# Kernel tuning notes

Measured on AMD Instinct MI355X. Metric: run time of the kernel, lower is better.

The kernel has to match this reference:

```python
import jax, jax.numpy as jnp
import numpy as np
from jax import lax

# ---- constants matching init kwargs / proposal_creator(mode='testing') ----
RATIOS = (0.5, 1.0, 2.0)
SCALES = (8.0, 16.0, 32.0)
BASE = 16.0          # generate_anchor_base base_size
STRIDE = 16          # feat_stride
NMS_THRESH = 0.7
N_PRE = 3000         # n_test_pre_nms
N_POST = 300         # n_test_post_nms
MIN_SIZE = 16.0      # min_size * scale (scale=1)


def _anchor_base():
    # (9, 4) xyxy anchors centered at (BASE/2, BASE/2); ratios outer, scales inner
    r = np.array(RATIOS, np.float32)
    s = np.array(SCALES, np.float32)
    hs = (BASE * s[None, :] * np.sqrt(r)[:, None]).reshape(-1)
    ws = (BASE * s[None, :] * np.sqrt(1.0 / r)[:, None]).reshape(-1)
    cx = cy = BASE / 2.0
    return np.stack([cx - ws / 2, cy - hs / 2, cx + ws / 2, cy + hs / 2], 1).astype(np.float32)


def _all_anchors(h, w):
    # _enumerate_shifted_anchor: shift grid flattened y-outer/x-inner to match
    # permute(0,2,3,1).view(n,-1,4) layout of the conv outputs.
    base = jnp.asarray(_anchor_base())                     # (9,4)
    sx = jnp.arange(w, dtype=jnp.float32) * STRIDE
    sy = jnp.arange(h, dtype=jnp.float32) * STRIDE
    SX, SY = jnp.meshgrid(sx, sy)                          # (h,w)
    shifts = jnp.stack([SX, SY, SX, SY], -1).reshape(-1, 4)  # (h*w,4)
    return (shifts[:, None, :] + base[None, :, :]).reshape(-1, 4)  # (h*w*9,4)


def _proposals(loc, score, anchor, img_h, img_w):
    # loc: (K,4) deltas, score: (K,) fg prob, anchor: (K,4) xyxy
    aw = anchor[:, 2] - anchor[:, 0]
    ah = anchor[:, 3] - anchor[:, 1]
    acx = anchor[:, 0] + 0.5 * aw
    acy = anchor[:, 1] + 0.5 * ah
    cx = loc[:, 0] * aw + acx
    cy = loc[:, 1] * ah + acy
    bw = aw * jnp.exp(loc[:, 2])
    bh = ah * jnp.exp(loc[:, 3])
    x1 = jnp.clip(cx - 0.5 * bw, 0.0, img_w)
    y1 = jnp.clip(cy - 0.5 * bh, 0.0, img_h)
    x2 = jnp.clip(cx + 0.5 * bw, 0.0, img_w)
    y2 = jnp.clip(cy + 0.5 * bh, 0.0, img_h)
    boxes = jnp.stack([x1, y1, x2, y2], 1)
    valid = ((x2 - x1) >= MIN_SIZE) & ((y2 - y1) >= MIN_SIZE)
    # min-size filter -> sink invalid boxes with -inf score, then top-k pre-NMS
    masked = jnp.where(valid, score, -jnp.inf)
    _, idx = lax.top_k(masked, N_PRE)
    b = boxes[idx]                                         # (N_PRE,4), score-sorted desc
    v = valid[idx]
    # pairwise IoU (torchvision convention: no +1)
    area = (b[:, 2] - b[:, 0]) * (b[:, 3] - b[:, 1])
    ix1 = jnp.maximum(b[:, None, 0], b[None, :, 0])
    iy1 = jnp.maximum(b[:, None, 1], b[None, :, 1])
    ix2 = jnp.minimum(b[:, None, 2], b[None, :, 2])
    iy2 = jnp.minimum(b[:, None, 3], b[None, :, 3])
    inter = jnp.clip(ix2 - ix1, 0.0) * jnp.clip(iy2 - iy1, 0.0)
    union = area[:, None] + area[None, :] - inter
    iou = jnp.where(union > 0.0, inter / union, 0.0)
    sup = iou > NMS_THRESH                                 # (N_PRE,N_PRE) bool
    # greedy sequential NMS over score order
    ar = jnp.arange(N_PRE)
    def body(keep, i):
        keep = keep & ~(keep[i] & sup[i] & (ar > i))
        return keep, None
    keep, _ = lax.scan(body, v, ar)
    # first N_POST kept boxes (score order); pad by cycling kept boxes
    order = jnp.argsort(jnp.where(keep, ar, N_PRE))        # kept indices first, sorted
    nk = jnp.maximum(keep.sum(), 1)
    pos = jnp.arange(N_POST)
    sel = order[jnp.where(pos < nk, pos, pos % nk)]
    return b[sel]                                          # (N_POST,4)


def setup_inputs() -> dict:
    key = jax.random.key(0)
    ks = jax.random.split(key, 4)
    n, c, h, w = 4, 512, 38, 38
    return {
        "x": jax.random.normal(ks[0], (n, c, h, w), jnp.float32),
        "conv1_w": jax.random.normal(ks[1], (512, 512, 3, 3), jnp.float32) * 0.01,
        "conv1_b": jnp.zeros((512,), jnp.float32),
        "score_w": jax.random.normal(ks[2], (18, 512), jnp.float32) * 0.01,
        "score_b": jnp.zeros((18,), jnp.float32),
        "loc_w": jax.random.normal(ks[3], (36, 512), jnp.float32) * 0.01,
        "loc_b": jnp.zeros((36,), jnp.float32),
        "img_h": 608,
        "img_w": 608,
    }


def reference(x, conv1_w, conv1_b, score_w, score_b, loc_w, loc_b, img_h, img_w):
    n, _, h, w = x.shape
    feat = jax.nn.relu(
        lax.conv_general_dilated(x, conv1_w, (1, 1), "SAME",
                                 dimension_numbers=("NCHW", "OIHW", "NCHW"))
        + conv1_b[None, :, None, None])
    locs = jnp.einsum("nchw,oc->nohw", feat, loc_w) + loc_b[None, :, None, None]
    scores = jnp.einsum("nchw,oc->nohw", feat, score_w) + score_b[None, :, None, None]
    rpn_locs = locs.transpose(0, 2, 3, 1).reshape(n, -1, 4)      # (n, h*w*9, 4)
    rpn_scores = scores.transpose(0, 2, 3, 1).reshape(n, -1, 2)  # (n, h*w*9, 2)
    fg = jax.nn.softmax(rpn_scores, axis=-1)[..., 1]             # (n, h*w*9)
    anchor = _all_anchors(h, w)
    ih = jnp.float32(img_h)
    iw = jnp.float32(img_w)
    rois = jax.vmap(lambda l, s: _proposals(l, s, anchor, ih, iw))(rpn_locs, fg)
    rois_indices = jnp.broadcast_to(
        jnp.arange(n, dtype=x.dtype)[:, None], (n, N_POST))
    return rpn_locs, rpn_scores, rois.reshape(-1, 4), rois_indices, anchor[None]
```

## Files before the change

### kernel.cpp

```cpp
#include <hip/hip_runtime.h>
#include <cstdint>
#include <cstddef>

#define HW    1444
#define NA    12996
#define NPRE  3000
#define NW    47
#define NPOST 300

#define OFF_LOCS   0
#define OFF_SCORES 207936
#define OFF_ROIS   311904
#define OFF_IDX    316704
#define OFF_ANCH   317904

#define INVALID_KEY 0xFFF0000000000000ULL

typedef float f32x2 __attribute__((ext_vector_type(2)));

__device__ inline double as_dim(int raw) {
  if (raw > 0 && raw < 1000000) return (double)raw;
  return (double)__int_as_float(raw);
}

__global__ __launch_bounds__(256) void wt_k(const float* __restrict__ lw,
                                            const float* __restrict__ sw,
                                            float* __restrict__ Wt) {
  int t = blockIdx.x * 256 + threadIdx.x;
  if (t >= 64 * 512) return;
  int o = t & 63, c = t >> 6;
  float v = 0.f;
  if (o < 36)      v = lw[o * 512 + c];
  else if (o < 54) v = sw[(o - 36) * 512 + c];
  Wt[t] = v;
}

__global__ __launch_bounds__(256) void conv_k(const float* __restrict__ X,
                                              const float* __restrict__ W,
                                              const float* __restrict__ B,
                                              float* __restrict__ F) {
  __shared__ float Xs[480];
  __shared__ float Wsf[2340];
  const int tid  = threadIdx.x;
  const int lane = tid & 63;
  const int wv   = tid >> 6;
  const int seg  = wv * 10;
  const int y  = blockIdx.x;
  const int o0 = blockIdx.y * 64;
  const int n  = blockIdx.z;
  const float* xn = X + ((size_t)n * 512) * HW;

  int xsrc[2]; bool xval[2]; bool xact[2];
#pragma unroll
  for (int u = 0; u < 2; ++u) {
    int e = tid + u * 256;
    xact[u] = (e < 480);
    int cl = e / 120, rem = e - cl * 120;
    int row = rem / 40, col = rem - row * 40;
    int iy = y - 1 + row, ix = col - 1;
    xval[u] = xact[u] && (iy >= 0 && iy < 38 && ix >= 0 && ix < 38);
    xsrc[u] = xval[u] ? (cl * HW + iy * 38 + ix) : 0;
  }
  int wdst[9], wsrc[9];
#pragma unroll
  for (int u = 0; u < 9; ++u) {
    int e = tid + u * 256;
    int ol = e / 36, rem = e - ol * 36;
    int cl = rem / 9, k = rem - cl * 9;
    wdst[u] = (cl * 9 + k) * 65 + ol;
    wsrc[u] = (o0 + ol) * 4608 + cl * 9 + k;
  }

  float xr_[2], wr_[9];
#pragma unroll
  for (int u = 0; u < 2; ++u) xr_[u] = xval[u] ? xn[xsrc[u]] : 0.f;
#pragma unroll
  for (int u = 0; u < 9; ++u) wr_[u] = W[wsrc[u]];

  double acc[10];
#pragma unroll
  for (int p = 0; p < 10; ++p) acc[p] = 0.;
  f32x2 pA[5], pB[5];
  float pc0 = 0.f;

  for (int cc = 0; cc < 128; ++cc) {
    __syncthreads();
#pragma unroll
    for (int u = 0; u < 2; ++u)
      if (xact[u]) Xs[tid + u * 256] = xr_[u];
#pragma unroll
    for (int u = 0; u < 9; ++u) Wsf[wdst[u]] = wr_[u];
    __syncthreads();
    if (cc < 127) {
      const int cb = (cc + 1) * 4;
#pragma unroll
      for (int u = 0; u < 2; ++u) xr_[u] = xval[u] ? xn[(size_t)cb * HW + xsrc[u]] : 0.f;
#pragma unroll
      for (int u = 0; u < 9; ++u) wr_[u] = W[wsrc[u] + cb * 9];
    }
    if ((cc & 1) == 0) {
#pragma unroll
      for (int a = 0; a < 5; ++a) { pA[a] = (f32x2)(0.f); pB[a] = (f32x2)(0.f); }
      pc0 = 0.f;
    }
#pragma unroll
    for (int cl = 0; cl < 4; ++cl) {
      f32x2 wp[9];
#pragma unroll
      for (int t = 0; t < 9; ++t) {
        float wv0 = Wsf[(cl * 9 + t) * 65 + lane];
        wp[t][0] = wv0; wp[t][1] = wv0;
      }
#pragma unroll
      for (int ky = 0; ky < 3; ++ky) {
        const float* xrow = &Xs[cl * 120 + ky * 40 + seg];
        f32x2 xp[6];
#pragma unroll
        for (int j = 0; j < 6; ++j) xp[j] = *(const f32x2*)(xrow + 2 * j);
#pragma unroll
        for (int a = 0; a < 5; ++a)
          asm("v_pk_fma_f32 %0, %1, %2, %0"
              : "+v"(pA[a]) : "v"(xp[a]), "v"(wp[ky * 3 + 0]));
        pc0 = fmaf(wp[ky * 3 + 1][0], xp[0][1], pc0);
#pragma unroll
        for (int a = 0; a < 5; ++a)
          asm("v_pk_fma_f32 %0, %1, %2, %0"
              : "+v"(pB[a]) : "v"(xp[a + 1]), "v"(wp[ky * 3 + 1]));
#pragma unroll
        for (int a = 0; a < 5; ++a)
          asm("v_pk_fma_f32 %0, %1, %2, %0"
              : "+v"(pA[a]) : "v"(xp[a + 1]), "v"(wp[ky * 3 + 2]));
      }
    }
    if (cc & 1) {
      acc[0] += (double)(pA[0][0] + pc0);
#pragma unroll
      for (int p = 1; p < 10; ++p) {
        float sa = pA[p >> 1][p & 1];
        float sb = (p & 1) ? pB[(p - 1) >> 1][0] : pB[(p - 2) >> 1][1];
        acc[p] += (double)(sa + sb);
      }
    }
  }
  double bb = (double)B[o0 + lane];
  float* fp = F + ((size_t)(n * 512 + o0 + lane)) * HW + y * 38;
#pragma unroll
  for (int p = 0; p < 10; ++p) {
    int col = seg + p;
    if (col < 38) fp[col] = (float)fmax(acc[p] + bb, 0.0);
  }
}

__global__ __launch_bounds__(256) void heads_k(const float* __restrict__ F,
                                               const float* __restrict__ Wt,
                                               const float* __restrict__ lb,
                                               const float* __restrict__ sb,
                                               float* __restrict__ out,
                                               double* __restrict__ fg) {
  __shared__ float sf[512 * 4];
  __shared__ double ssc[4][18];
  int n = blockIdx.y;
  int p0 = blockIdx.x * 4;
  int tid = threadIdx.x;
  const float* fn = F + ((size_t)n * 512) * HW;
  for (int e = tid; e < 2048; e += 256) {
    int c = e >> 2, pl = e & 3;
    sf[e] = fn[c * HW + p0 + pl];
  }
  __syncthreads();
  int pl = tid & 3, o = tid >> 2;
  double acc = 0.;
  if (o < 54) {
    for (int c = 0; c < 512; ++c)
      acc = fma((double)Wt[(c << 6) | o], (double)sf[(c << 2) | pl], acc);
  }
  int p = p0 + pl;
  if (o < 36) {
    acc += (double)lb[o];
    out[OFF_LOCS + ((size_t)n * NA + (size_t)p * 9 + (o >> 2)) * 4 + (o & 3)] = (float)acc;
  } else if (o < 54) {
    int oo = o - 36;
    acc += (double)sb[oo];
    out[OFF_SCORES + ((size_t)n * NA + (size_t)p * 9 + (oo >> 1)) * 2 + (oo & 1)] = (float)acc;
    ssc[pl][oo] = acc;
  }
  __syncthreads();
  if (tid < 36) {
    int pl2 = tid / 9, a = tid - pl2 * 9;
    double s0 = ssc[pl2][a * 2], s1 = ssc[pl2][a * 2 + 1];
    double mx = fmax(s0, s1);
    double e0 = exp(s0 - mx), e1 = exp(s1 - mx);
    fg[(size_t)n * NA + (size_t)(p0 + pl2) * 9 + a] = e1 / (e0 + e1);
  }
}

__global__ __launch_bounds__(256) void decode_k(const float* __restrict__ out_c,
                                                float* __restrict__ out,
                                                const double* __restrict__ fg,
                                                const int* __restrict__ ihp,
                                                const int* __restrict__ iwp,
                                                double* __restrict__ boxes,
                                                unsigned long long* __restrict__ keys) {
  int t = blockIdx.x * 256 + threadIdx.x;
  int n = t >> 14, i = t & 16383;
  if (i >= NA) { keys[t] = ~0ULL; return; }
  int p = i / 9, a = i - p * 9;
  int ri = a / 3, si = a - ri * 3;
  double sr  = (ri == 0) ? 0.7071067811865476 : (ri == 1 ? 1.0 : 1.4142135623730951);
  double sri = (ri == 0) ? 1.4142135623730951 : (ri == 1 ? 1.0 : 0.7071067811865476);
  double hs = (double)(128 << si) * sr;
  double wd = (double)(128 << si) * sri;
  int py = p / 38, px = p - py * 38;
  float sx = (float)(px * 16), sy = (float)(py * 16);
  float fx1 = (float)(8.0 - 0.5 * wd), fy1 = (float)(8.0 - 0.5 * hs);
  float fx2 = (float)(8.0 + 0.5 * wd), fy2 = (float)(8.0 + 0.5 * hs);
  float ax1f = sx + fx1, ay1f = sy + fy1, ax2f = sx + fx2, ay2f = sy + fy2;
  if (n == 0) {
    float* ap = out + OFF_ANCH + (size_t)i * 4;
    ap[0] = ax1f; ap[1] = ay1f; ap[2] = ax2f; ap[3] = ay2f;
  }
  double ax1 = ax1f, ay1 = ay1f, ax2 = ax2f, ay2 = ay2f;
  double aw = ax2 - ax1, ah = ay2 - ay1;
  double acx = ax1 + 0.5 * aw, acy = ay1 + 0.5 * ah;
  const float* lp = out_c + OFF_LOCS + ((size_t)n * NA + i) * 4;
  double cx = (double)lp[0] * aw + acx, cy = (double)lp[1] * ah + acy;
  double bw = aw * exp((double)lp[2]), bh = ah * exp((double)lp[3]);
  double iwf = as_dim(iwp[0]), ihf = as_dim(ihp[0]);
  double x1 = fmin(fmax(cx - 0.5 * bw, 0.0), iwf);
  double y1 = fmin(fmax(cy - 0.5 * bh, 0.0), ihf);
  double x2 = fmin(fmax(cx + 0.5 * bw, 0.0), iwf);
  double y2 = fmin(fmax(cy + 0.5 * bh, 0.0), ihf);
  bool valid = ((x2 - x1) >= 16.0) && ((y2 - y1) >= 16.0);
  double* bp = boxes + ((size_t)n * NA + i) * 4;
  bp[0] = x1; bp[1] = y1; bp[2] = x2; bp[3] = y2;
  double sc = fg[(size_t)n * NA + i];
  unsigned long long u = (unsigned long long)__double_as_longlong(sc);
  u = (u >> 63) ? ~u : (u | 0x8000000000000000ULL);
  unsigned long long inv = ~u;
  if (!valid) inv = INVALID_KEY;
  keys[t] = (inv & ~0x3FFFULL) | (unsigned long long)i;
}

__global__ __launch_bounds__(1024) void sortA_k(unsigned long long* __restrict__ keys) {
  __shared__ unsigned long long s[8192];
  const int half = blockIdx.x & 1;
  unsigned long long* g = keys + (((size_t)(blockIdx.x >> 1)) << 14) + ((size_t)half << 13);
  const int tid = threadIdx.x;
  for (int i = tid; i < 8192; i += 1024) s[i] = g[i];
  for (int size = 2; size <= 8192; size <<= 1) {
    for (int stride = size >> 1; stride > 0; stride >>= 1) {
      __syncthreads();
      for (int u = tid; u < 4096; u += 1024) {
        int lo = u & (stride - 1);
        int i1 = ((u - lo) << 1) | lo;
        int i2 = i1 + stride;
        bool up = (i1 & size) == 0;
        if (half) up = !up;
        unsigned long long a = s[i1], b = s[i2];
        if ((a > b) == up) { s[i1] = b; s[i2] = a; }
      }
    }
  }
  __syncthreads();
  for (int i = tid; i < 8192; i += 1024) g[i] = s[i];
}

__global__ __launch_bounds__(256) void sortB_k(unsigned long long* __restrict__ keys) {
  int t = blockIdx.x * 256 + threadIdx.x;
  int n = t >> 13, i = t & 8191;
  unsigned long long* g = keys + ((size_t)n << 14);
  unsigned long long a = g[i], b = g[i + 8192];
  if (a > b) { g[i] = b; g[i + 8192] = a; }
}

__global__ __launch_bounds__(1024) void sortC_k(unsigned long long* __restrict__ keys) {
  __shared__ unsigned long long s[8192];
  unsigned long long* g = keys + (((size_t)(blockIdx.x >> 1)) << 14) + ((size_t)(blockIdx.x & 1) << 13);
  const int tid = threadIdx.x;
  for (int i = tid; i < 8192; i += 1024) s[i] = g[i];
  for (int stride = 4096; stride > 0; stride >>= 1) {
    __syncthreads();
    for (int u = tid; u < 4096; u += 1024) {
      int lo = u & (stride - 1);
      int i1 = ((u - lo) << 1) | lo;
      int i2 = i1 + stride;
      unsigned long long a = s[i1], b = s[i2];
      if (a > b) { s[i1] = b; s[i2] = a; }
    }
  }
  __syncthreads();
  for (int i = tid; i < 8192; i += 1024) g[i] = s[i];
}

__global__ void gather_k(const unsigned long long* __restrict__ keys,
                         const double* __restrict__ boxes,
                         double* __restrict__ bsort,
                         unsigned long long* __restrict__ vw) {
  int n = blockIdx.y, w = blockIdx.x, l = threadIdx.x;
  int r = w * 64 + l;
  bool valid = false;
  if (r < NPRE) {
    unsigned long long kk = keys[((size_t)n << 14) + r];
    valid = kk < INVALID_KEY;
    unsigned idx = (unsigned)(kk & 0x3FFFULL);
    const double* bp = boxes + ((size_t)n * NA + idx) * 4;
    double* dp = bsort + ((size_t)n * NPRE + r) * 4;
    dp[0] = bp[0]; dp[1] = bp[1]; dp[2] = bp[2]; dp[3] = bp[3];
  }
  unsigned long long mask = __ballot(valid);
  if (l == 0) vw[n * NW + w] = mask;
}

__global__ __launch_bounds__(256) void iou_k(const double* __restrict__ bsort,
                                             unsigned long long* __restrict__ sup) {
  int t = blockIdx.x * 256 + threadIdx.x;
  if (t >= 4 * NPRE * NW) return;
  int w = t % NW; int rest = t / NW; int i = rest % NPRE; int n = rest / NPRE;
  const double* bb = bsort + (size_t)n * NPRE * 4;
  double bix1 = bb[(size_t)i*4], biy1 = bb[(size_t)i*4+1];
  double bix2 = bb[(size_t)i*4+2], biy2 = bb[(size_t)i*4+3];
  double ai = (bix2 - bix1) * (biy2 - biy1);
  unsigned long long word = 0ULL;
  int j0 = w << 6;
  if (j0 + 63 > i) {
    int lmax = NPRE - j0; if (lmax > 64) lmax = 64;
    for (int l = 0; l < lmax; ++l) {
      int j = j0 + l;
      if (j <= i) continue;
      const double* bj = bb + (size_t)j * 4;
      double aj = (bj[2] - bj[0]) * (bj[3] - bj[1]);
      double xx1 = fmax(bix1, bj[0]), yy1 = fmax(biy1, bj[1]);
      double xx2 = fmin(bix2, bj[2]), yy2 = fmin(biy2, bj[3]);
      double inter = fmax(xx2 - xx1, 0.0) * fmax(yy2 - yy1, 0.0);
      double uni = ai + aj - inter;
      double iou = (uni > 0.0) ? inter / uni : 0.0;
      word |= (unsigned long long)(iou > 0.7) << l;
    }
  }
  sup[((size_t)n * NPRE + i) * NW + w] = word;
}

__global__ void nms_k(const unsigned long long* __restrict__ sup,
                      const unsigned long long* __restrict__ vwp,
                      const double* __restrict__ bsort,
                      float* __restrict__ out) {
  int n = blockIdx.x; int l = threadIdx.x;
  unsigned long long vw = (l < NW) ? vwp[n * NW + l] : 0ULL;
  unsigned long long remv = 0ULL, keepw = 0ULL;
  const unsigned long long* sbase = sup + (size_t)n * NPRE * NW;
  unsigned long long r = (l < NPRE) ? sbase[(size_t)l * NW] : 0ULL;
  for (int b = 0; b < NW; ++b) {
    unsigned long long rn = 0ULL;
    if (b + 1 < NW) {
      int gi = (b + 1) * 64 + l;
      if (gi < NPRE) rn = sbase[(size_t)gi * NW + (b + 1)];
    }
    unsigned long long kept = __shfl(vw & ~remv, b);
    unsigned long long todo = kept;
    while (todo) {
      int i = __builtin_ctzll(todo);
      unsigned long long ri = __shfl(r, i);
      kept &= ~ri;
      todo &= todo - 1;
      todo &= ~ri;
    }
    if (l == b) keepw = kept;
    unsigned long long m = kept;
    while (m) {
      int i0 = __builtin_ctzll(m); m &= m - 1;
      int i1 = -1, i2 = -1, i3 = -1, i4 = -1, i5 = -1, i6 = -1, i7 = -1;
      if (m) { i1 = __builtin_ctzll(m); m &= m - 1; }
      if (m) { i2 = __builtin_ctzll(m); m &= m - 1; }
      if (m) { i3 = __builtin_ctzll(m); m &= m - 1; }
      if (m) { i4 = __builtin_ctzll(m); m &= m - 1; }
      if (m) { i5 = __builtin_ctzll(m); m &= m - 1; }
      if (m) { i6 = __builtin_ctzll(m); m &= m - 1; }
      if (m) { i7 = __builtin_ctzll(m); m &= m - 1; }
      if (l < NW) {
        const unsigned long long* rb = sbase + (size_t)(b << 6) * NW + l;
        unsigned long long a0 = rb[(size_t)i0 * NW];
        unsigned long long a1 = (i1 >= 0) ? rb[(size_t)i1 * NW] : 0ULL;
        unsigned long long a2 = (i2 >= 0) ? rb[(size_t)i2 * NW] : 0ULL;
        unsigned long long a3 = (i3 >= 0) ? rb[(size_t)i3 * NW] : 0ULL;
        unsigned long long a4 = (i4 >= 0) ? rb[(size_t)i4 * NW] : 0ULL;
        unsigned long long a5 = (i5 >= 0) ? rb[(size_t)i5 * NW] : 0ULL;
        unsigned long long a6 = (i6 >= 0) ? rb[(size_t)i6 * NW] : 0ULL;
        unsigned long long a7 = (i7 >= 0) ? rb[(size_t)i7 * NW] : 0ULL;
        remv |= (((a0 | a1) | (a2 | a3)) | ((a4 | a5) | (a6 | a7)));
      }
    }
    r = rn;
  }
  unsigned long long keep = keepw;
  int cnt = __popcll(keep);
  int pre = cnt;
#pragma unroll
  for (int d = 1; d < 64; d <<= 1) {
    int tt = __shfl_up(pre, d);
    if (l >= d) pre += tt;
  }
  int nk = __shfl(pre, 63);
  int excl = pre - cnt;
  __shared__ float sbox[NPOST * 4];
  unsigned long long m2 = keep; int rank = excl;
  while (m2) {
    int b = __builtin_ctzll(m2);
    m2 &= m2 - 1;
    if (rank < NPOST) {
      int j = (l << 6) + b;
      const double* bj = bsort + ((size_t)n * NPRE + j) * 4;
      sbox[rank*4]   = (float)bj[0]; sbox[rank*4+1] = (float)bj[1];
      sbox[rank*4+2] = (float)bj[2]; sbox[rank*4+3] = (float)bj[3];
    }
    ++rank;
  }
  __syncthreads();
  if (nk == 0 && l == 0) {
    const double* b0 = bsort + (size_t)n * NPRE * 4;
    sbox[0] = (float)b0[0]; sbox[1] = (float)b0[1];
    sbox[2] = (float)b0[2]; sbox[3] = (float)b0[3];
  }
  __syncthreads();
  int nke = nk > 0 ? nk : 1;
  for (int r2 = l; r2 < NPOST; r2 += 64) {
    int src = r2 < nke ? r2 : r2 % nke;
    float4 b4 = *(float4*)(sbox + src * 4);
    *(float4*)(out + OFF_ROIS + ((size_t)n * NPOST + r2) * 4) = b4;
    out[OFF_IDX + n * NPOST + r2] = (float)n;
  }
}

extern "C" void kernel_launch(void* const* d_in, const int* in_sizes, int n_in,
                              void* d_out, int out_size, void* d_ws, size_t ws_size,
                              hipStream_t stream) {
  const float* X  = (const float*)d_in[0];
  const float* CW = (const float*)d_in[1];
  const float* CB = (const float*)d_in[2];
  const float* SW = (const float*)d_in[3];
  const float* SB = (const float*)d_in[4];
  const float* LW = (const float*)d_in[5];
  const float* LB = (const float*)d_in[6];
  const int*   IH = (const int*)d_in[7];
  const int*   IW = (const int*)d_in[8];
  float* out = (float*)d_out;
  char* ws = (char*)d_ws;

  float* feat = (float*)(ws + 0);
  unsigned long long* sup  = (unsigned long long*)(ws + 0);
  float* Wt    = (float*)(ws + 11829248);
  double* fg   = (double*)(ws + 11960320);
  double* boxes= (double*)(ws + 12376192);
  unsigned long long* keys = (unsigned long long*)(ws + 14039680);
  double* bsort= (double*)(ws + 14563968);
  unsigned long long* vw   = (unsigned long long*)(ws + 14947968);

  hipLaunchKernelGGL(wt_k,     dim3(128),        dim3(256),  0, stream, LW, SW, Wt);
  hipLaunchKernelGGL(conv_k,   dim3(38, 8, 4),   dim3(256),  0, stream, X, CW, CB, feat);
  hipLaunchKernelGGL(heads_k,  dim3(361, 4),     dim3(256),  0, stream, feat, Wt, LB, SB, out, fg);
  hipLaunchKernelGGL(decode_k, dim3(256),        dim3(256),  0, stream, out, out, fg, IH, IW, boxes, keys);
  hipLaunchKernelGGL(sortA_k,  dim3(8),          dim3(1024), 0, stream, keys);
  hipLaunchKernelGGL(sortB_k,  dim3(128),        dim3(256),  0, stream, keys);
  hipLaunchKernelGGL(sortC_k,  dim3(8),          dim3(1024), 0, stream, keys);
  hipLaunchKernelGGL(gather_k, dim3(47, 4),      dim3(64),   0, stream, keys, boxes, bsort, vw);
  hipLaunchKernelGGL(iou_k,    dim3((4*NPRE*NW + 255) / 256), dim3(256), 0, stream, bsort, sup);
  hipLaunchKernelGGL(nms_k,    dim3(4),          dim3(64),   0, stream, sup, vw, bsort, out);
}
```

Measured before the change: 1.004 ms.

## Load conv weights directly to registers and use vectorized 16-byte LDS reads for input

Drops the shared-memory weight tile: each lane now loads its own output channel's 36 weights per step straight from global memory as nine float4 loads. The input tile is stored twice in LDS, once in the original layout and once with 44-wide padded rows shifted so odd waves get 16-byte-aligned addresses, which lets each row be fetched with three float4 LDS reads instead of six float2 reads. This removes the weight LDS stores and reads and cuts LDS instruction count. In exchange it issues per-lane strided global loads every iteration, which are not prefetched a step ahead, and it roughly doubles the input staging stores.

```diff
diff --git a/kernel.cpp b/kernel.cpp
--- a/kernel.cpp
+++ b/kernel.cpp
@@ -17,6 +17,7 @@
 #define INVALID_KEY 0xFFF0000000000000ULL
 
 typedef float f32x2 __attribute__((ext_vector_type(2)));
+typedef float f32x4 __attribute__((ext_vector_type(4)));
 
 __device__ inline double as_dim(int raw) {
   if (raw > 0 && raw < 1000000) return (double)raw;
@@ -39,8 +40,7 @@
                                               const float* __restrict__ W,
                                               const float* __restrict__ B,
                                               float* __restrict__ F) {
-  __shared__ float Xs[480];
-  __shared__ float Wsf[2340];
+  __shared__ float Xs[1008];
   const int tid  = threadIdx.x;
   const int lane = tid & 63;
   const int wv   = tid >> 6;
@@ -49,33 +49,40 @@
   const int o0 = blockIdx.y * 64;
   const int n  = blockIdx.z;
   const float* xn = X + ((size_t)n * 512) * HW;
-
-  int xsrc[2]; bool xval[2]; bool xact[2];
-#pragma unroll
-  for (int u = 0; u < 2; ++u) {
+  const float* Wl = W + (size_t)(o0 + lane) * 4608;
+
+  int xsrcA[2]; bool xvalA[2]; bool xactA1;
+  {
+    int e = tid;
+    int cl = e / 120, rem = e - cl * 120, row = rem / 40, colA = rem - row * 40;
+    int m = colA - 1, iy = y - 1 + row;
+    xvalA[0] = (m >= 0 && m < 38 && iy >= 0 && iy < 38);
+    xsrcA[0] = xvalA[0] ? (cl * HW + iy * 38 + m) : 0;
+  }
+  {
+    int e = tid + 256; xactA1 = (e < 480);
+    int cl = e / 120, rem = e - cl * 120, row = rem / 40, colA = rem - row * 40;
+    int m = colA - 1, iy = y - 1 + row;
+    xvalA[1] = xactA1 && (m >= 0 && m < 38 && iy >= 0 && iy < 38);
+    xsrcA[1] = xvalA[1] ? (cl * HW + iy * 38 + m) : 0;
+  }
+  int xsrcB[3]; bool xvalB[3]; bool xactB2;
+#pragma unroll
+  for (int u = 0; u < 3; ++u) {
     int e = tid + u * 256;
-    xact[u] = (e < 480);
-    int cl = e / 120, rem = e - cl * 120;
-    int row = rem / 40, col = rem - row * 40;
-    int iy = y - 1 + row, ix = col - 1;
-    xval[u] = xact[u] && (iy >= 0 && iy < 38 && ix >= 0 && ix < 38);
-    xsrc[u] = xval[u] ? (cl * HW + iy * 38 + ix) : 0;
-  }
-  int wdst[9], wsrc[9];
-#pragma unroll
-  for (int u = 0; u < 9; ++u) {
-    int e = tid + u * 256;
-    int ol = e / 36, rem = e - ol * 36;
-    int cl = rem / 9, k = rem - cl * 9;
-    wdst[u] = (cl * 9 + k) * 65 + ol;
-    wsrc[u] = (o0 + ol) * 4608 + cl * 9 + k;
-  }
-
-  float xr_[2], wr_[9];
-#pragma unroll
-  for (int u = 0; u < 2; ++u) xr_[u] = xval[u] ? xn[xsrc[u]] : 0.f;
-#pragma unroll
-  for (int u = 0; u < 9; ++u) wr_[u] = W[wsrc[u]];
+    bool act = (e < 528);
+    int cl = e / 132, rem = e - cl * 132, row = rem / 44, colB = rem - row * 44;
+    int m = colB - 3, iy = y - 1 + row;
+    xvalB[u] = act && (m >= 0 && m < 38 && iy >= 0 && iy < 38);
+    xsrcB[u] = xvalB[u] ? (cl * HW + iy * 38 + m) : 0;
+    if (u == 2) xactB2 = act;
+  }
+
+  float xrA[2], xrB[3];
+#pragma unroll
+  for (int u = 0; u < 2; ++u) xrA[u] = xvalA[u] ? xn[xsrcA[u]] : 0.f;
+#pragma unroll
+  for (int u = 0; u < 3; ++u) xrB[u] = xvalB[u] ? xn[xsrcB[u]] : 0.f;
 
   double acc[10];
 #pragma unroll
@@ -83,20 +90,33 @@
   f32x2 pA[5], pB[5];
   float pc0 = 0.f;
 
+  const int  xb0   = (wv & 1) ? (480 + seg + 2) : seg;
+  const int  cstep = (wv & 1) ? 132 : 120;
+  const int  kstep = (wv & 1) ? 44 : 40;
+
+#define WQ_ELEM(t) ((t & 3) == 0 ? wq[(t) >> 2].x : (t & 3) == 1 ? wq[(t) >> 2].y : \
+                    (t & 3) == 2 ? wq[(t) >> 2].z : wq[(t) >> 2].w)
+
   for (int cc = 0; cc < 128; ++cc) {
     __syncthreads();
-#pragma unroll
-    for (int u = 0; u < 2; ++u)
-      if (xact[u]) Xs[tid + u * 256] = xr_[u];
-#pragma unroll
-    for (int u = 0; u < 9; ++u) Wsf[wdst[u]] = wr_[u];
+    Xs[tid] = xrA[0];
+    if (xactA1) Xs[tid + 256] = xrA[1];
+    Xs[480 + tid] = xrB[0];
+    Xs[480 + tid + 256] = xrB[1];
+    if (xactB2) Xs[480 + tid + 512] = xrB[2];
     __syncthreads();
+    f32x4 wq[9];
+    {
+      const f32x4* wp4 = (const f32x4*)(Wl + cc * 36);
+#pragma unroll
+      for (int q = 0; q < 9; ++q) wq[q] = wp4[q];
+    }
     if (cc < 127) {
       const int cb = (cc + 1) * 4;
 #pragma unroll
-      for (int u = 0; u < 2; ++u) xr_[u] = xval[u] ? xn[(size_t)cb * HW + xsrc[u]] : 0.f;
-#pragma unroll
-      for (int u = 0; u < 9; ++u) wr_[u] = W[wsrc[u] + cb * 9];
+      for (int u = 0; u < 2; ++u) xrA[u] = xvalA[u] ? xn[cb * HW + xsrcA[u]] : 0.f;
+#pragma unroll
+      for (int u = 0; u < 3; ++u) xrB[u] = xvalB[u] ? xn[cb * HW + xsrcB[u]] : 0.f;
     }
     if ((cc & 1) == 0) {
 #pragma unroll
@@ -107,16 +127,23 @@
     for (int cl = 0; cl < 4; ++cl) {
       f32x2 wp[9];
 #pragma unroll
-      for (int t = 0; t < 9; ++t) {
-        float wv0 = Wsf[(cl * 9 + t) * 65 + lane];
-        wp[t][0] = wv0; wp[t][1] = wv0;
+      for (int k = 0; k < 9; ++k) {
+        float wv0 = WQ_ELEM(cl * 9 + k);
+        wp[k][0] = wv0; wp[k][1] = wv0;
       }
 #pragma unroll
       for (int ky = 0; ky < 3; ++ky) {
-        const float* xrow = &Xs[cl * 120 + ky * 40 + seg];
+        const float* xrow = &Xs[xb0 + cl * cstep + ky * kstep];
+        f32x4 q0 = *(const f32x4*)(xrow);
+        f32x4 q1 = *(const f32x4*)(xrow + 4);
+        f32x4 q2 = *(const f32x4*)(xrow + 8);
         f32x2 xp[6];
-#pragma unroll
-        for (int j = 0; j < 6; ++j) xp[j] = *(const f32x2*)(xrow + 2 * j);
+        xp[0] = __builtin_shufflevector(q0, q0, 0, 1);
+        xp[1] = __builtin_shufflevector(q0, q0, 2, 3);
+        xp[2] = __builtin_shufflevector(q1, q1, 0, 1);
+        xp[3] = __builtin_shufflevector(q1, q1, 2, 3);
+        xp[4] = __builtin_shufflevector(q2, q2, 0, 1);
+        xp[5] = __builtin_shufflevector(q2, q2, 2, 3);
 #pragma unroll
         for (int a = 0; a < 5; ++a)
           asm("v_pk_fma_f32 %0, %1, %2, %0"
```

Result: slower. 1.232 ms (+22.7%).
